# Kernel optimization log

Hardware: AMD Instinct MI355X
Metric: run time of the kernel (lower is better)

Reference implementation:

```python
import jax, jax.numpy as jnp
import numpy as np

N = 50000      # num nodes
E = 600000     # num edges
D = 128        # num_node_features (in == out)
R = 8          # num_relations


def setup_inputs() -> dict:
    key = jax.random.key(0)
    k = jax.random.split(key, 6)
    x = jax.random.normal(k[0], (N, D), dtype=jnp.float32)
    edge_index = jax.random.randint(k[1], (2, E), 0, N, dtype=jnp.int32)
    edge_type = jax.random.randint(k[2], (E,), 0, R, dtype=jnp.int32)
    scale = 1.0 / np.sqrt(D).astype(np.float32)
    weight = jax.random.normal(k[3], (R, D, D), dtype=jnp.float32) * scale  # per-relation W_r
    root = jax.random.normal(k[4], (D, D), dtype=jnp.float32) * scale       # self-loop weight
    bias = jnp.zeros((D,), dtype=jnp.float32)
    return {"x": x, "edge_index": edge_index, "edge_type": edge_type,
            "weight": weight, "root": root, "bias": bias}


def _rgcn(x, weight, root, bias, edge_index, edge_type):
    # RGCNConv (PyG defaults: aggr='mean' per relation, root weight + bias)
    src, dst = edge_index[0], edge_index[1]
    # combined segment id over (relation, dst) so one segment_sum covers all relations
    seg = edge_type * N + dst                              # [E]
    msgs = x[src]                                          # [E, D] gather
    sums = jax.ops.segment_sum(msgs, seg, num_segments=R * N)                 # [R*N, D]
    cnts = jax.ops.segment_sum(jnp.ones((E, 1), x.dtype), seg, num_segments=R * N)
    mean = sums / jnp.maximum(cnts, 1.0)                   # mean over neighbors, 0 if none
    agg = mean.reshape(R, N, D)
    out = jnp.einsum('rnd,rde->ne', agg, weight) + x @ root + bias
    return out


def reference(x, edge_index, edge_type, weight, root, bias):
    return jax.nn.relu(_rgcn(x, weight, root, bias, edge_index, edge_type))
```

## Files before the change

kernel.cpp:

```cpp
#include <hip/hip_runtime.h>

constexpr int NN = 50000;
constexpr int NE = 600000;
constexpr int D  = 128;
constexpr int NR = 8;
constexpr int KT = (NR + 1) * D;
constexpr int NSEG = NN * NR;

constexpr int SCAN_ELEMS = 1024;
constexpr int NBLK2 = (NSEG + SCAN_ELEMS - 1) / SCAN_ELEMS;

typedef unsigned int   u32;
typedef unsigned short u16;
typedef float  f32x4 __attribute__((ext_vector_type(4)));
typedef short  s16x8 __attribute__((ext_vector_type(8)));

__device__ __forceinline__ u16 f2bf(float f) {
    u32 u = __float_as_uint(f);
    u32 r = (u + 0x7fffu + ((u >> 16) & 1u)) >> 16;
    return (u16)r;
}

__device__ __forceinline__ void async_cp16(const void* g, void* l) {
    __builtin_amdgcn_global_load_lds(
        (const __attribute__((address_space(1))) u32*)g,
        (__attribute__((address_space(3))) u32*)l, 16, 0, 0);
}

__global__ __launch_bounds__(256) void prep_all(const float* __restrict__ x,
                                                const float* __restrict__ weight,
                                                const float* __restrict__ root,
                                                const int* __restrict__ dst,
                                                const int* __restrict__ et,
                                                u16* __restrict__ xb,
                                                u16* __restrict__ wt,
                                                u16* __restrict__ rt,
                                                int* __restrict__ cnt2) {
    const int NX4 = NN * D / 4;
    const int NW  = (NR + 1) * D * D;
    int gid = blockIdx.x * 256 + threadIdx.x;
    if (gid < NX4) {
        int i = gid * 4;
        float4 v = *(const float4*)(x + i);
        ushort4 o;
        o.x = f2bf(v.x); o.y = f2bf(v.y); o.z = f2bf(v.z); o.w = f2bf(v.w);
        *(ushort4*)(xb + i) = o;
        return;
    }
    int g = gid - NX4;
    if (g < NW) {
        int p = g >> 14;
        int idx = g & 16383;
        int n = idx >> 7, k = idx & 127;
        float v = (p < NR) ? weight[(size_t)p * D * D + k * D + n] : root[k * D + n];
        u16* dp = (p < NR) ? (wt + (size_t)p * D * D) : rt;
        dp[idx] = f2bf(v);
        return;
    }
    int e = g - NW;
    if (e < NE) atomicAdd(&cnt2[dst[e] * NR + et[e]], 1);
}

__global__ __launch_bounds__(256) void scan1(const int* __restrict__ cnt,
                                             int* __restrict__ offs,
                                             int* __restrict__ bsums) {
    __shared__ int lds[256];
    int t = threadIdx.x;
    int base = blockIdx.x * SCAN_ELEMS + t * 4;
    int v0 = (base + 0 < NSEG) ? cnt[base + 0] : 0;
    int v1 = (base + 1 < NSEG) ? cnt[base + 1] : 0;
    int v2 = (base + 2 < NSEG) ? cnt[base + 2] : 0;
    int v3 = (base + 3 < NSEG) ? cnt[base + 3] : 0;
    int s = v0 + v1 + v2 + v3;
    lds[t] = s;
    __syncthreads();
    int val = s;
    for (int off = 1; off < 256; off <<= 1) {
        int tmp = (t >= off) ? lds[t - off] : 0;
        __syncthreads();
        val += tmp;
        lds[t] = val;
        __syncthreads();
    }
    int ex = val - s;
    if (base + 0 < NSEG) offs[base + 0] = ex;
    if (base + 1 < NSEG) offs[base + 1] = ex + v0;
    if (base + 2 < NSEG) offs[base + 2] = ex + v0 + v1;
    if (base + 3 < NSEG) offs[base + 3] = ex + v0 + v1 + v2;
    if (t == 255) bsums[blockIdx.x] = val;
}

__global__ __launch_bounds__(512) void scan2(int* __restrict__ bsums) {
    __shared__ int lds[512];
    int t = threadIdx.x;
    int v = (t < NBLK2) ? bsums[t] : 0;
    lds[t] = v;
    __syncthreads();
    int val = v;
    for (int off = 1; off < 512; off <<= 1) {
        int tmp = (t >= off) ? lds[t - off] : 0;
        __syncthreads();
        val += tmp;
        lds[t] = val;
        __syncthreads();
    }
    if (t < NBLK2) bsums[t] = val - v;
}

__global__ __launch_bounds__(256) void scan3(int* __restrict__ offs,
                                             int* __restrict__ cur,
                                             const int* __restrict__ bsums) {
    int i = blockIdx.x * 256 + threadIdx.x;
    if (i < NSEG) {
        int v = offs[i] + bsums[i >> 10];
        offs[i] = v;
        cur[i]  = v;
    }
    if (i == 0) offs[NSEG] = NE;
}

__global__ __launch_bounds__(256) void fill_bins(const int* __restrict__ src,
                                                 const int* __restrict__ dst,
                                                 const int* __restrict__ et,
                                                 int* __restrict__ cur,
                                                 int* __restrict__ ebin) {
    int e = blockIdx.x * 256 + threadIdx.x;
    if (e >= NE) return;
    int r = et[e];
    int idx = atomicAdd(&cur[dst[e] * NR + r], 1);
    ebin[idx] = (r << 16) | src[e];
}

__global__ __launch_bounds__(128) void aggregate_kernel(const u32* __restrict__ xw,
                                                        const int* __restrict__ offs2,
                                                        const int* __restrict__ ebin,
                                                        u32* __restrict__ sw) {
    const int lane = threadIdx.x & 63;
    const int n = blockIdx.x * 2 + (threadIdx.x >> 6);
    if (n >= NN) return;
    const int beg = __builtin_amdgcn_readfirstlane(offs2[n * NR]);
    const int c   = __builtin_amdgcn_readfirstlane(offs2[n * NR + NR]) - beg;

    float a0 = 0.f, a1 = 0.f;
    int r_cur = 0, cnt_cur = 0;

    int q0 = 0, q1 = 0, q2 = 0, q3 = 0, q4 = 0, q5 = 0, q6 = 0, q7 = 0;
    u32 v0 = 0, v1 = 0, v2 = 0, v3 = 0, v4 = 0, v5 = 0, v6 = 0, v7 = 0;

#define REFILL(Q, V, IDX)                                                   \
    if ((IDX) < c) {                                                        \
        Q = __builtin_amdgcn_readfirstlane(ebin[beg + (IDX)]);              \
        V = xw[(size_t)((u32)Q & 0xffffu) * 64 + lane];                     \
    }
#define FLUSH()                                                             \
    {                                                                       \
        float inv_ = 1.0f / (float)(cnt_cur > 0 ? cnt_cur : 1);             \
        u32 lo16_ = f2bf(a0 * inv_);                                        \
        u32 hi16_ = f2bf(a1 * inv_);                                        \
        sw[((size_t)r_cur * NN + n) * 64 + lane] = lo16_ | (hi16_ << 16);   \
        a0 = 0.f; a1 = 0.f; cnt_cur = 0; ++r_cur;                           \
    }
#define CONSUME(Q, V)                                                       \
    {                                                                       \
        int rj_ = (int)((u32)(Q) >> 16);                                    \
        while (r_cur < rj_) FLUSH()                                         \
        a0 += __uint_as_float((V) << 16);                                   \
        a1 += __uint_as_float((V) & 0xffff0000u);                           \
        ++cnt_cur;                                                          \
    }

    REFILL(q0, v0, 0) REFILL(q1, v1, 1) REFILL(q2, v2, 2) REFILL(q3, v3, 3)
    REFILL(q4, v4, 4) REFILL(q5, v5, 5) REFILL(q6, v6, 6) REFILL(q7, v7, 7)

    int e = 0;
    for (; e + 8 <= c; e += 8) {
        CONSUME(q0, v0) REFILL(q0, v0, e + 8)
        CONSUME(q1, v1) REFILL(q1, v1, e + 9)
        CONSUME(q2, v2) REFILL(q2, v2, e + 10)
        CONSUME(q3, v3) REFILL(q3, v3, e + 11)
        CONSUME(q4, v4) REFILL(q4, v4, e + 12)
        CONSUME(q5, v5) REFILL(q5, v5, e + 13)
        CONSUME(q6, v6) REFILL(q6, v6, e + 14)
        CONSUME(q7, v7) REFILL(q7, v7, e + 15)
    }
    if (e + 0 < c) CONSUME(q0, v0)
    if (e + 1 < c) CONSUME(q1, v1)
    if (e + 2 < c) CONSUME(q2, v2)
    if (e + 3 < c) CONSUME(q3, v3)
    if (e + 4 < c) CONSUME(q4, v4)
    if (e + 5 < c) CONSUME(q5, v5)
    if (e + 6 < c) CONSUME(q6, v6)
    if (e + 7 < c) CONSUME(q7, v7)

    while (r_cur < NR) FLUSH()
#undef REFILL
#undef FLUSH
#undef CONSUME
}

__global__ __launch_bounds__(256) void mfma_gemm(const u16* __restrict__ xb,
                                                 const u16* __restrict__ sums,
                                                 const u16* __restrict__ rt,
                                                 const u16* __restrict__ wt,
                                                 const float* __restrict__ bias,
                                                 float* __restrict__ out) {
    __shared__ u16 As[64 * 32];
    __shared__ u16 Bs[128 * 32];

    const int tid  = threadIdx.x;
    const int wave = tid >> 6;
    const int lane = tid & 63;
    const int m0   = blockIdx.x * 64;

    f32x4 acc[8];
#pragma unroll
    for (int j = 0; j < 8; ++j) acc[j] = (f32x4){0.f, 0.f, 0.f, 0.f};

    const int srow = 16 * wave + (lane >> 2);
    const int sch  = (lane & 3) * 8;

    for (int k0 = 0; k0 < KT; k0 += 32) {
        const int rpl = k0 >> 7;
        const int kof = k0 & 127;
        const u16* Ap = (rpl == 0) ? xb : sums + (size_t)(rpl - 1) * NN * D;
        const u16* Bp = (rpl == 0) ? rt : wt + (size_t)(rpl - 1) * D * D;

        __syncthreads();
        {
            int ga = m0 + srow; if (ga > NN - 1) ga = NN - 1;
            async_cp16(Ap + (size_t)ga * D + kof + sch, (char*)As + wave * 1024);
            async_cp16(Bp + (size_t)srow * D + kof + sch, (char*)Bs + wave * 1024);
            async_cp16(Bp + (size_t)(64 + srow) * D + kof + sch,
                       (char*)Bs + 4096 + wave * 1024);
        }
        __syncthreads();

        const int fr = lane & 15;
        const int fk = (lane >> 4) * 8;
        s16x8 af = *(const s16x8*)&As[(16 * wave + fr) * 32 + fk];
#pragma unroll
        for (int nt = 0; nt < 8; ++nt) {
            s16x8 bf = *(const s16x8*)&Bs[(nt * 16 + fr) * 32 + fk];
            acc[nt] = __builtin_amdgcn_mfma_f32_16x16x32_bf16(af, bf, acc[nt], 0, 0, 0);
        }
    }

    const int cl = lane & 15;
    const int rq = (lane >> 4) * 4;
#pragma unroll
    for (int nt = 0; nt < 8; ++nt) {
        int col = nt * 16 + cl;
        float bv = bias[col];
#pragma unroll
        for (int reg = 0; reg < 4; ++reg) {
            int n = m0 + 16 * wave + rq + reg;
            if (n < NN) {
                float v = acc[nt][reg] + bv;
                out[(size_t)n * D + col] = fmaxf(v, 0.0f);
            }
        }
    }
}

extern "C" void kernel_launch(void* const* d_in, const int* in_sizes, int n_in,
                              void* d_out, int out_size, void* d_ws, size_t ws_size,
                              hipStream_t stream) {
    const float* x      = (const float*)d_in[0];
    const int*   ei     = (const int*)d_in[1];
    const int*   et     = (const int*)d_in[2];
    const float* weight = (const float*)d_in[3];
    const float* root   = (const float*)d_in[4];
    const float* bias   = (const float*)d_in[5];
    float* out = (float*)d_out;
    const int* srcv = ei;
    const int* dstv = ei + NE;

    int* cnt2  = (int*)d_ws;
    int* cur2  = cnt2 + NSEG;
    int* offs2 = cur2 + NSEG;
    int* bsums = offs2 + NSEG + 1;
    int* ebin  = bsums + 512;
    size_t fixed_b  = ((char*)(ebin + NE) - (char*)d_ws);
    size_t fixed_al = (fixed_b + 255) & ~(size_t)255;
    u16* xb   = (u16*)((char*)d_ws + fixed_al);
    u16* sums = xb + (size_t)NN * D;
    u16* wt   = sums + (size_t)NR * NN * D;
    u16* rt   = wt + (size_t)NR * D * D;

    hipMemsetAsync(cnt2, 0, NSEG * sizeof(int), stream);

    const int PREP = NN * D / 4 + (NR + 1) * D * D + NE;
    prep_all<<<(PREP + 255) / 256, 256, 0, stream>>>(x, weight, root, dstv, et,
                                                     xb, wt, rt, cnt2);

    scan1<<<NBLK2, 256, 0, stream>>>(cnt2, offs2, bsums);
    scan2<<<1, 512, 0, stream>>>(bsums);
    scan3<<<(NSEG + 256) / 256, 256, 0, stream>>>(offs2, cur2, bsums);
    fill_bins<<<(NE + 255) / 256, 256, 0, stream>>>(srcv, dstv, et, cur2, ebin);

    aggregate_kernel<<<(NN + 1) / 2, 128, 0, stream>>>((const u32*)xb, offs2, ebin,
                                                       (u32*)sums);

    mfma_gemm<<<(NN + 63) / 64, 256, 0, stream>>>(xb, sums, rt, wt, bias, out);
}
```

Measured before the change: 220.0 us.

## Fuse neighbor aggregation into MFMA GEMM with relation-major CSR binning

Merges the aggregation and GEMM kernels into one kernel. Each 128-node block aggregates relation r's neighbor means straight into LDS, then multiplies them against that relation's weight tile, so the 8×N×D bf16 sums buffer never goes to global memory. Segments become relation-major so each wave walks a contiguous edge range per relation. The kernel also uses larger 128x128 tiles with swizzled B loads and nontemporal output stores. The cost is much larger LDS use per block, which lowers occupancy, and aggregation and MFMA work are serialized within each block.

Measured after the change: 273.8 us. 24.5% more time.

```diff
diff --git a/kernel.cpp b/kernel.cpp
--- a/kernel.cpp
+++ b/kernel.cpp
@@ -4,8 +4,7 @@
 constexpr int NE = 600000;
 constexpr int D  = 128;
 constexpr int NR = 8;
-constexpr int KT = (NR + 1) * D;
-constexpr int NSEG = NN * NR;
+constexpr int NSEG = NR * NN;
 
 constexpr int SCAN_ELEMS = 1024;
 constexpr int NBLK2 = (NSEG + SCAN_ELEMS - 1) / SCAN_ELEMS;
@@ -51,14 +50,14 @@
     if (g < NW) {
         int p = g >> 14;
         int idx = g & 16383;
-        int n = idx >> 7, k = idx & 127;
-        float v = (p < NR) ? weight[(size_t)p * D * D + k * D + n] : root[k * D + n];
+        int c = idx >> 7, k = idx & 127;
+        float v = (p < NR) ? weight[(size_t)p * D * D + k * D + c] : root[k * D + c];
         u16* dp = (p < NR) ? (wt + (size_t)p * D * D) : rt;
         dp[idx] = f2bf(v);
         return;
     }
     int e = g - NW;
-    if (e < NE) atomicAdd(&cnt2[dst[e] * NR + et[e]], 1);
+    if (e < NE) atomicAdd(&cnt2[et[e] * NN + dst[e]], 1);
 }
 
 __global__ __launch_bounds__(256) void scan1(const int* __restrict__ cnt,
@@ -126,30 +125,71 @@
                                                  int* __restrict__ ebin) {
     int e = blockIdx.x * 256 + threadIdx.x;
     if (e >= NE) return;
-    int r = et[e];
-    int idx = atomicAdd(&cur[dst[e] * NR + r], 1);
-    ebin[idx] = (r << 16) | src[e];
-}
-
-__global__ __launch_bounds__(128) void aggregate_kernel(const u32* __restrict__ xw,
-                                                        const int* __restrict__ offs2,
-                                                        const int* __restrict__ ebin,
-                                                        u32* __restrict__ sw) {
-    const int lane = threadIdx.x & 63;
-    const int n = blockIdx.x * 2 + (threadIdx.x >> 6);
-    if (n >= NN) return;
-    const int beg = __builtin_amdgcn_readfirstlane(offs2[n * NR]);
-    const int c   = __builtin_amdgcn_readfirstlane(offs2[n * NR + NR]) - beg;
-
-    float a0 = 0.f, a1 = 0.f;
-    int r_cur = 0, cnt_cur = 0;
-
-    int q0 = 0, q1 = 0, q2 = 0, q3 = 0, q4 = 0, q5 = 0, q6 = 0, q7 = 0;
-    u32 v0 = 0, v1 = 0, v2 = 0, v3 = 0, v4 = 0, v5 = 0, v6 = 0, v7 = 0;
+    int d = dst[e];
+    int idx = atomicAdd(&cur[et[e] * NN + d], 1);
+    ebin[idx] = (int)(((u32)d << 16) | (u32)src[e]);
+}
+
+__global__ __launch_bounds__(256) void fused_kernel(const u32* __restrict__ xw,
+                                                    const u16* __restrict__ wt,
+                                                    const u16* __restrict__ rt,
+                                                    const int* __restrict__ offs,
+                                                    const int* __restrict__ ebin,
+                                                    const float* __restrict__ bias,
+                                                    float* __restrict__ out) {
+    __shared__ u16 As[128 * 136];
+    __shared__ u16 Bs[128 * 128];
+
+    const int tid  = threadIdx.x;
+    const int wave = tid >> 6;
+    const int lane = tid & 63;
+    const int m0   = blockIdx.x * 128;
+    const int wm   = (wave & 1) * 64;
+    const int wn   = (wave >> 1) * 64;
+    const int fr   = lane & 15;
+    const int fq   = lane >> 4;
+    u32* Asw = (u32*)As;
+
+    int node_lo = m0 + wave * 32; if (node_lo > NN) node_lo = NN;
+    int node_hi = node_lo + 32;   if (node_hi > NN) node_hi = NN;
+
+    f32x4 acc[4][4];
+#pragma unroll
+    for (int i = 0; i < 4; ++i)
+#pragma unroll
+        for (int j = 0; j < 4; ++j) acc[i][j] = (f32x4){0.f, 0.f, 0.f, 0.f};
+
+    for (int p = 0; p <= NR; ++p) {
+        const u16* Bp = (p == 0) ? rt : wt + (size_t)(p - 1) * D * D;
+#pragma unroll
+        for (int j = 0; j < 8; ++j) {
+            int gcid = j * 256 + tid;
+            int col  = gcid >> 4;
+            int gch  = (gcid & 15) ^ (col & 15);
+            async_cp16(Bp + col * D + gch * 8,
+                       (char*)Bs + (size_t)(j * 256 + wave * 64) * 16);
+        }
+
+        if (p == 0) {
+            for (int n = node_lo; n < node_hi; n += 8) {
+                u32 vv[8];
+                int lim = node_hi - n; if (lim > 8) lim = 8;
+                for (int j = 0; j < lim; ++j) vv[j] = xw[(size_t)(n + j) * 64 + lane];
+                for (int j = 0; j < lim; ++j) Asw[(n + j - m0) * 68 + lane] = vv[j];
+            }
+        } else {
+            const int r = p - 1;
+            const int lo = __builtin_amdgcn_readfirstlane(offs[r * NN + node_lo]);
+            const int c  = __builtin_amdgcn_readfirstlane(offs[r * NN + node_hi]) - lo;
+            float a0 = 0.f, a1 = 0.f;
+            int cnt_cur = 0, n_cur = node_lo;
+
+            int q0 = 0, q1 = 0, q2 = 0, q3 = 0, q4 = 0, q5 = 0, q6 = 0, q7 = 0;
+            u32 v0 = 0, v1 = 0, v2 = 0, v3 = 0, v4 = 0, v5 = 0, v6 = 0, v7 = 0;
 
 #define REFILL(Q, V, IDX)                                                   \
     if ((IDX) < c) {                                                        \
-        Q = __builtin_amdgcn_readfirstlane(ebin[beg + (IDX)]);              \
+        Q = __builtin_amdgcn_readfirstlane(ebin[lo + (IDX)]);               \
         V = xw[(size_t)((u32)Q & 0xffffu) * 64 + lane];                     \
     }
 #define FLUSH()                                                             \
@@ -157,106 +197,84 @@
         float inv_ = 1.0f / (float)(cnt_cur > 0 ? cnt_cur : 1);             \
         u32 lo16_ = f2bf(a0 * inv_);                                        \
         u32 hi16_ = f2bf(a1 * inv_);                                        \
-        sw[((size_t)r_cur * NN + n) * 64 + lane] = lo16_ | (hi16_ << 16);   \
-        a0 = 0.f; a1 = 0.f; cnt_cur = 0; ++r_cur;                           \
+        Asw[(n_cur - m0) * 68 + lane] = lo16_ | (hi16_ << 16);              \
+        a0 = 0.f; a1 = 0.f; cnt_cur = 0; ++n_cur;                           \
     }
 #define CONSUME(Q, V)                                                       \
     {                                                                       \
-        int rj_ = (int)((u32)(Q) >> 16);                                    \
-        while (r_cur < rj_) FLUSH()                                         \
+        int dn_ = (int)((u32)(Q) >> 16);                                    \
+        while (n_cur < dn_) FLUSH()                                         \
         a0 += __uint_as_float((V) << 16);                                   \
         a1 += __uint_as_float((V) & 0xffff0000u);                           \
         ++cnt_cur;                                                          \
     }
-
-    REFILL(q0, v0, 0) REFILL(q1, v1, 1) REFILL(q2, v2, 2) REFILL(q3, v3, 3)
-    REFILL(q4, v4, 4) REFILL(q5, v5, 5) REFILL(q6, v6, 6) REFILL(q7, v7, 7)
-
-    int e = 0;
-    for (; e + 8 <= c; e += 8) {
-        CONSUME(q0, v0) REFILL(q0, v0, e + 8)
-        CONSUME(q1, v1) REFILL(q1, v1, e + 9)
-        CONSUME(q2, v2) REFILL(q2, v2, e + 10)
-        CONSUME(q3, v3) REFILL(q3, v3, e + 11)
-        CONSUME(q4, v4) REFILL(q4, v4, e + 12)
-        CONSUME(q5, v5) REFILL(q5, v5, e + 13)
-        CONSUME(q6, v6) REFILL(q6, v6, e + 14)
-        CONSUME(q7, v7) REFILL(q7, v7, e + 15)
-    }
-    if (e + 0 < c) CONSUME(q0, v0)
-    if (e + 1 < c) CONSUME(q1, v1)
-    if (e + 2 < c) CONSUME(q2, v2)
-    if (e + 3 < c) CONSUME(q3, v3)
-    if (e + 4 < c) CONSUME(q4, v4)
-    if (e + 5 < c) CONSUME(q5, v5)
-    if (e + 6 < c) CONSUME(q6, v6)
-    if (e + 7 < c) CONSUME(q7, v7)
-
-    while (r_cur < NR) FLUSH()
+            REFILL(q0, v0, 0) REFILL(q1, v1, 1) REFILL(q2, v2, 2) REFILL(q3, v3, 3)
+            REFILL(q4, v4, 4) REFILL(q5, v5, 5) REFILL(q6, v6, 6) REFILL(q7, v7, 7)
+            int e = 0;
+            for (; e + 8 <= c; e += 8) {
+                CONSUME(q0, v0) REFILL(q0, v0, e + 8)
+                CONSUME(q1, v1) REFILL(q1, v1, e + 9)
+                CONSUME(q2, v2) REFILL(q2, v2, e + 10)
+                CONSUME(q3, v3) REFILL(q3, v3, e + 11)
+                CONSUME(q4, v4) REFILL(q4, v4, e + 12)
+                CONSUME(q5, v5) REFILL(q5, v5, e + 13)
+                CONSUME(q6, v6) REFILL(q6, v6, e + 14)
+                CONSUME(q7, v7) REFILL(q7, v7, e + 15)
+            }
+            if (e + 0 < c) CONSUME(q0, v0)
+            if (e + 1 < c) CONSUME(q1, v1)
+            if (e + 2 < c) CONSUME(q2, v2)
+            if (e + 3 < c) CONSUME(q3, v3)
+            if (e + 4 < c) CONSUME(q4, v4)
+            if (e + 5 < c) CONSUME(q5, v5)
+            if (e + 6 < c) CONSUME(q6, v6)
+            if (e + 7 < c) CONSUME(q7, v7)
+            while (n_cur < node_hi) FLUSH()
 #undef REFILL
 #undef FLUSH
 #undef CONSUME
-}
-
-__global__ __launch_bounds__(256) void mfma_gemm(const u16* __restrict__ xb,
-                                                 const u16* __restrict__ sums,
-                                                 const u16* __restrict__ rt,
-                                                 const u16* __restrict__ wt,
-                                                 const float* __restrict__ bias,
-                                                 float* __restrict__ out) {
-    __shared__ u16 As[64 * 32];
-    __shared__ u16 Bs[128 * 32];
-
-    const int tid  = threadIdx.x;
-    const int wave = tid >> 6;
-    const int lane = tid & 63;
-    const int m0   = blockIdx.x * 64;
-
-    f32x4 acc[8];
-#pragma unroll
-    for (int j = 0; j < 8; ++j) acc[j] = (f32x4){0.f, 0.f, 0.f, 0.f};
-
-    const int srow = 16 * wave + (lane >> 2);
-    const int sch  = (lane & 3) * 8;
-
-    for (int k0 = 0; k0 < KT; k0 += 32) {
-        const int rpl = k0 >> 7;
-        const int kof = k0 & 127;
-        const u16* Ap = (rpl == 0) ? xb : sums + (size_t)(rpl - 1) * NN * D;
-        const u16* Bp = (rpl == 0) ? rt : wt + (size_t)(rpl - 1) * D * D;
-
-        __syncthreads();
-        {
-            int ga = m0 + srow; if (ga > NN - 1) ga = NN - 1;
-            async_cp16(Ap + (size_t)ga * D + kof + sch, (char*)As + wave * 1024);
-            async_cp16(Bp + (size_t)srow * D + kof + sch, (char*)Bs + wave * 1024);
-            async_cp16(Bp + (size_t)(64 + srow) * D + kof + sch,
-                       (char*)Bs + 4096 + wave * 1024);
         }
-        __syncthreads();
-
-        const int fr = lane & 15;
-        const int fk = (lane >> 4) * 8;
-        s16x8 af = *(const s16x8*)&As[(16 * wave + fr) * 32 + fk];
-#pragma unroll
-        for (int nt = 0; nt < 8; ++nt) {
-            s16x8 bf = *(const s16x8*)&Bs[(nt * 16 + fr) * 32 + fk];
-            acc[nt] = __builtin_amdgcn_mfma_f32_16x16x32_bf16(af, bf, acc[nt], 0, 0, 0);
+
+        __syncthreads();
+
+#pragma unroll
+        for (int kk = 0; kk < 4; ++kk) {
+            const int ch = kk * 4 + fq;
+            s16x8 af[4], bf[4];
+#pragma unroll
+            for (int mt = 0; mt < 4; ++mt)
+                af[mt] = *(const s16x8*)&As[(wm + mt * 16 + fr) * 136 + ch * 8];
+#pragma unroll
+            for (int nt = 0; nt < 4; ++nt) {
+                int col = wn + nt * 16 + fr;
+                int pos = ch ^ (col & 15);
+                bf[nt] = *(const s16x8*)&Bs[col * 128 + pos * 8];
+            }
+#pragma unroll
+            for (int mt = 0; mt < 4; ++mt)
+#pragma unroll
+                for (int nt = 0; nt < 4; ++nt)
+                    acc[mt][nt] = __builtin_amdgcn_mfma_f32_16x16x32_bf16(
+                        af[mt], bf[nt], acc[mt][nt], 0, 0, 0);
         }
+        __syncthreads();
     }
 
     const int cl = lane & 15;
     const int rq = (lane >> 4) * 4;
 #pragma unroll
-    for (int nt = 0; nt < 8; ++nt) {
-        int col = nt * 16 + cl;
+    for (int nt = 0; nt < 4; ++nt) {
+        int col = wn + nt * 16 + cl;
         float bv = bias[col];
 #pragma unroll
-        for (int reg = 0; reg < 4; ++reg) {
-            int n = m0 + 16 * wave + rq + reg;
-            if (n < NN) {
-                float v = acc[nt][reg] + bv;
-                out[(size_t)n * D + col] = fmaxf(v, 0.0f);
+        for (int mt = 0; mt < 4; ++mt) {
+#pragma unroll
+            for (int reg = 0; reg < 4; ++reg) {
+                int n = m0 + wm + mt * 16 + rq + reg;
+                if (n < NN) {
+                    float v = fmaxf(acc[mt][nt][reg] + bv, 0.0f);
+                    __builtin_nontemporal_store(v, &out[(size_t)n * D + col]);
+                }
             }
         }
     }
@@ -282,10 +300,9 @@
     int* ebin  = bsums + 512;
     size_t fixed_b  = ((char*)(ebin + NE) - (char*)d_ws);
     size_t fixed_al = (fixed_b + 255) & ~(size_t)255;
-    u16* xb   = (u16*)((char*)d_ws + fixed_al);
-    u16* sums = xb + (size_t)NN * D;
-    u16* wt   = sums + (size_t)NR * NN * D;
-    u16* rt   = wt + (size_t)NR * D * D;
+    u16* xb = (u16*)((char*)d_ws + fixed_al);
+    u16* wt = xb + (size_t)NN * D;
+    u16* rt = wt + (size_t)NR * D * D;
 
     hipMemsetAsync(cnt2, 0, NSEG * sizeof(int), stream);
 
@@ -298,8 +315,6 @@
     scan3<<<(NSEG + 256) / 256, 256, 0, stream>>>(offs2, cur2, bsums);
     fill_bins<<<(NE + 255) / 256, 256, 0, stream>>>(srcv, dstv, et, cur2, ebin);
 
-    aggregate_kernel<<<(NN + 1) / 2, 128, 0, stream>>>((const u32*)xb, offs2, ebin,
-                                                       (u32*)sums);
-
-    mfma_gemm<<<(NN + 63) / 64, 256, 0, stream>>>(xb, sums, rt, wt, bias, out);
-}
+    fused_kernel<<<(NN + 127) / 128, 256, 0, stream>>>((const u32*)xb, wt, rt,
+                                                       offs2, ebin, bias, out);
+}
```

## Pre-pack weights into MFMA fragment layout and load operands directly without LDS

Applied to the files above, without the earlier changes.

The weight and root matrices are now packed during prep into a chunked layout that matches the MFMA B-fragment order. The GEMM drops LDS staging and its two barriers per k-step, loading A rows and B fragments straight from global memory into registers. This removes the synchronization and LDS round-trip cost. In exchange every wave re-reads the full B matrix from global/L2 rather than sharing it through LDS, and there is no software prefetch.

Measured after the change: 242.5 us. 1.1x slower.

```diff
diff --git a/kernel.cpp b/kernel.cpp
--- a/kernel.cpp
+++ b/kernel.cpp
@@ -4,7 +4,6 @@
 constexpr int NE = 600000;
 constexpr int D  = 128;
 constexpr int NR = 8;
-constexpr int KT = (NR + 1) * D;
 constexpr int NSEG = NN * NR;
 
 constexpr int SCAN_ELEMS = 1024;
@@ -19,12 +18,6 @@
     u32 u = __float_as_uint(f);
     u32 r = (u + 0x7fffu + ((u >> 16) & 1u)) >> 16;
     return (u16)r;
-}
-
-__device__ __forceinline__ void async_cp16(const void* g, void* l) {
-    __builtin_amdgcn_global_load_lds(
-        (const __attribute__((address_space(1))) u32*)g,
-        (__attribute__((address_space(3))) u32*)l, 16, 0, 0);
 }
 
 __global__ __launch_bounds__(256) void prep_all(const float* __restrict__ x,
@@ -33,8 +26,7 @@
                                                 const int* __restrict__ dst,
                                                 const int* __restrict__ et,
                                                 u16* __restrict__ xb,
-                                                u16* __restrict__ wt,
-                                                u16* __restrict__ rt,
+                                                u16* __restrict__ bpk,
                                                 int* __restrict__ cnt2) {
     const int NX4 = NN * D / 4;
     const int NW  = (NR + 1) * D * D;
@@ -51,10 +43,10 @@
     if (g < NW) {
         int p = g >> 14;
         int idx = g & 16383;
-        int n = idx >> 7, k = idx & 127;
-        float v = (p < NR) ? weight[(size_t)p * D * D + k * D + n] : root[k * D + n];
-        u16* dp = (p < NR) ? (wt + (size_t)p * D * D) : rt;
-        dp[idx] = f2bf(v);
+        int c = idx >> 7, k = idx & 127;
+        float v  = (p < NR) ? weight[(size_t)p * D * D + k * D + c] : root[k * D + c];
+        int   dp = (p < NR) ? (p + 1) : 0;
+        bpk[(((size_t)dp * 16 + (k >> 3)) * 128 + c) * 8 + (k & 7)] = f2bf(v);
         return;
     }
     int e = g - NW;
@@ -200,56 +192,43 @@
 
 __global__ __launch_bounds__(256) void mfma_gemm(const u16* __restrict__ xb,
                                                  const u16* __restrict__ sums,
-                                                 const u16* __restrict__ rt,
-                                                 const u16* __restrict__ wt,
+                                                 const u16* __restrict__ bpk,
                                                  const float* __restrict__ bias,
                                                  float* __restrict__ out) {
-    __shared__ u16 As[64 * 32];
-    __shared__ u16 Bs[128 * 32];
-
     const int tid  = threadIdx.x;
     const int wave = tid >> 6;
     const int lane = tid & 63;
+    const int fr   = lane & 15;
+    const int fq   = lane >> 4;
     const int m0   = blockIdx.x * 64;
 
+    int row = m0 + wave * 16 + fr;
+    if (row > NN - 1) row = NN - 1;
+    const size_t arow = (size_t)row * D;
+
     f32x4 acc[8];
 #pragma unroll
     for (int j = 0; j < 8; ++j) acc[j] = (f32x4){0.f, 0.f, 0.f, 0.f};
 
-    const int srow = 16 * wave + (lane >> 2);
-    const int sch  = (lane & 3) * 8;
-
-    for (int k0 = 0; k0 < KT; k0 += 32) {
-        const int rpl = k0 >> 7;
-        const int kof = k0 & 127;
-        const u16* Ap = (rpl == 0) ? xb : sums + (size_t)(rpl - 1) * NN * D;
-        const u16* Bp = (rpl == 0) ? rt : wt + (size_t)(rpl - 1) * D * D;
-
-        __syncthreads();
-        {
-            int ga = m0 + srow; if (ga > NN - 1) ga = NN - 1;
-            async_cp16(Ap + (size_t)ga * D + kof + sch, (char*)As + wave * 1024);
-            async_cp16(Bp + (size_t)srow * D + kof + sch, (char*)Bs + wave * 1024);
-            async_cp16(Bp + (size_t)(64 + srow) * D + kof + sch,
-                       (char*)Bs + 4096 + wave * 1024);
+    for (int p = 0; p <= NR; ++p) {
+        const u16* Ap = ((p == 0) ? xb : sums + (size_t)(p - 1) * NN * D) + arow;
+        const u16* Bp = bpk + (size_t)p * 16 * 128 * 8;
+#pragma unroll
+        for (int kk = 0; kk < 4; ++kk) {
+            const int ch = kk * 4 + fq;
+            s16x8 af = *(const s16x8*)(Ap + ch * 8);
+#pragma unroll
+            for (int nt = 0; nt < 8; ++nt) {
+                s16x8 bf = *(const s16x8*)(Bp + ((size_t)ch * 128 + nt * 16 + fr) * 8);
+                acc[nt] = __builtin_amdgcn_mfma_f32_16x16x32_bf16(af, bf, acc[nt], 0, 0, 0);
+            }
         }
-        __syncthreads();
-
-        const int fr = lane & 15;
-        const int fk = (lane >> 4) * 8;
-        s16x8 af = *(const s16x8*)&As[(16 * wave + fr) * 32 + fk];
-#pragma unroll
-        for (int nt = 0; nt < 8; ++nt) {
-            s16x8 bf = *(const s16x8*)&Bs[(nt * 16 + fr) * 32 + fk];
-            acc[nt] = __builtin_amdgcn_mfma_f32_16x16x32_bf16(af, bf, acc[nt], 0, 0, 0);
-        }
-    }
-
-    const int cl = lane & 15;
-    const int rq = (lane >> 4) * 4;
+    }
+
+    const int rq = fq * 4;
 #pragma unroll
     for (int nt = 0; nt < 8; ++nt) {
-        int col = nt * 16 + cl;
+        int col = nt * 16 + fr;
         float bv = bias[col];
 #pragma unroll
         for (int reg = 0; reg < 4; ++reg) {
@@ -284,14 +263,13 @@
     size_t fixed_al = (fixed_b + 255) & ~(size_t)255;
     u16* xb   = (u16*)((char*)d_ws + fixed_al);
     u16* sums = xb + (size_t)NN * D;
-    u16* wt   = sums + (size_t)NR * NN * D;
-    u16* rt   = wt + (size_t)NR * D * D;
+    u16* bpk  = sums + (size_t)NR * NN * D;
 
     hipMemsetAsync(cnt2, 0, NSEG * sizeof(int), stream);
 
     const int PREP = NN * D / 4 + (NR + 1) * D * D + NE;
     prep_all<<<(PREP + 255) / 256, 256, 0, stream>>>(x, weight, root, dstv, et,
-                                                     xb, wt, rt, cnt2);
+                                                     xb, bpk, cnt2);
 
     scan1<<<NBLK2, 256, 0, stream>>>(cnt2, offs2, bsums);
     scan2<<<1, 512, 0, stream>>>(bsums);
@@ -301,5 +279,5 @@
     aggregate_kernel<<<(NN + 1) / 2, 128, 0, stream>>>((const u32*)xb, offs2, ebin,
                                                        (u32*)sums);
 
-    mfma_gemm<<<(NN + 63) / 64, 256, 0, stream>>>(xb, sums, rt, wt, bias, out);
-}
+    mfma_gemm<<<(NN + 63) / 64, 256, 0, stream>>>(xb, sums, bpk, bias, out);
+}
```
